# Kernel optimization log

Measured on AMD Instinct MI355X. Metric: run time of the kernel, lower is better.

The kernel has to match this reference:

```python
import jax, jax.numpy as jnp
import numpy as np

C = 32  # channel dim ('size' in the torch module)


def setup_inputs() -> dict:
    key = jax.random.key(0)
    ks = jax.random.split(key, 9)
    B, H, W = 8, 64, 512
    shape = (B, C, H, W)
    q = jax.random.normal(ks[0], shape, dtype=jnp.float32)
    k = jax.random.normal(ks[1], shape, dtype=jnp.float32)
    v = jax.random.normal(ks[2], shape, dtype=jnp.float32)
    s = 1.0 / np.sqrt(C)  # kaiming-uniform-ish scale for 1x1 conv
    wq = jax.random.uniform(ks[3], (C, C), jnp.float32, -s, s)
    bq = jax.random.uniform(ks[4], (C,), jnp.float32, -s, s)
    wk = jax.random.uniform(ks[5], (C, C), jnp.float32, -s, s)
    bk = jax.random.uniform(ks[6], (C,), jnp.float32, -s, s)
    wv = jax.random.uniform(ks[7], (C, C), jnp.float32, -s, s)
    bv = jax.random.uniform(ks[8], (C,), jnp.float32, -s, s)
    return {"q": q, "k": k, "v": v, "wq": wq, "bq": bq,
            "wk": wk, "bk": bk, "wv": wv, "bv": bv}


def _proj(x, w, b):
    # 1x1 conv on NCHW == per-pixel linear over channels; emit NHWC directly
    return jnp.einsum('oc,bchw->bhwo', w, x) + b


def reference(q, k, v, wq, bq, wk, bk, wv, bv):
    residual = q  # [B,C,H,W]
    qp = _proj(q, wq, bq)  # [B,H,W,C]
    kp = _proj(k, wk, bk)
    vp = _proj(v, wv, bv)
    # unnormalized attention over the W axis, batched over (B,H)
    attn = jnp.einsum('bhwc,bhxc->bhwx', qp, kp)        # [B,H,W,W]
    att = jnp.einsum('bhwx,bhxc->bhwc', attn, vp)       # [B,H,W,C]
    out = jnp.transpose(att, (0, 3, 1, 2)) + residual   # back to NCHW
    return out
```

## Files before the change

kernel.cpp:

```cpp
#include <hip/hip_runtime.h>
#include <hip/hip_bf16.h>

#define CH   32
#define WD   512
#define NH   64
#define CHST (NH * WD)
#define BST  (CH * CHST)
#define NST  36

typedef short bf16x8 __attribute__((ext_vector_type(8)));
typedef float f32x16 __attribute__((ext_vector_type(16)));
typedef float f32x8  __attribute__((ext_vector_type(8)));

__device__ __forceinline__ unsigned short f2bf(float f) {
  union { __hip_bfloat16 h; unsigned short u; } cv;
  cv.h = __float2bfloat16(f);
  return cv.u;
}
__device__ __forceinline__ float bf2f(unsigned short u) {
  return __uint_as_float(((unsigned int)u) << 16);
}
__device__ __forceinline__ unsigned int pk2(float lo_, float hi_) {
  return ((unsigned int)f2bf(hi_) << 16) | (unsigned int)f2bf(lo_);
}
__device__ __forceinline__ void swap32(unsigned int& a, unsigned int& b) {
  asm volatile("v_permlane32_swap_b32 %0, %1" : "+v"(a), "+v"(b));
}
union W4 { unsigned int u[4]; bf16x8 v; };

__device__ __forceinline__ void d2frag(const f32x16& d, W4& f0, W4& f1) {
  f0.u[0] = pk2(d[0], d[1]);   f0.u[1] = pk2(d[2],  d[3]);
  f0.u[2] = pk2(d[4], d[5]);   f0.u[3] = pk2(d[6],  d[7]);
  swap32(f0.u[0], f0.u[2]);    swap32(f0.u[1], f0.u[3]);
  f1.u[0] = pk2(d[8], d[9]);   f1.u[1] = pk2(d[10], d[11]);
  f1.u[2] = pk2(d[12], d[13]); f1.u[3] = pk2(d[14], d[15]);
  swap32(f1.u[0], f1.u[2]);    swap32(f1.u[1], f1.u[3]);
}
__device__ __forceinline__ float halfsum(float v) {
  return v + __shfl_xor(v, 32, 64);
}

__global__ __launch_bounds__(512, 4)
void fused_mha(const float* __restrict__ qg, const float* __restrict__ kg,
               const float* __restrict__ vg,
               const float* __restrict__ wqg, const float* __restrict__ bqg,
               const float* __restrict__ wkg, const float* __restrict__ bkg,
               const float* __restrict__ wvg, const float* __restrict__ bvg,
               float* __restrict__ outg)
{
  __shared__ float np[8][CH][NST];
  __shared__ float sp[8][2][CH];

  const int t = threadIdx.x, lane = t & 63, wid = t >> 6;
  const int lo = lane & 31, hi = lane >> 5;
  const int bh = blockIdx.x;
  const size_t base = (size_t)(bh >> 6) * BST + (size_t)(bh & 63) * WD;

  int rowr[16];
  #pragma unroll
  for (int r = 0; r < 16; ++r) rowr[r] = (r & 3) + 8 * (r >> 2) + 4 * hi;

  const float* krow = kg + base + (size_t)lo * CHST + 64 * wid + 8 * hi;
  const float* vrow = vg + base + (size_t)lo * CHST + 64 * wid + 8 * hi;
  f32x8 kf[4], vf[4];
  #pragma unroll
  for (int kk = 0; kk < 4; ++kk) {
    kf[kk] = *(const f32x8*)(krow + 16 * kk);
    vf[kk] = *(const f32x8*)(vrow + 16 * kk);
  }
  float qpf[32];
  #pragma unroll
  for (int it = 0; it < 2; ++it)
    #pragma unroll
    for (int s = 0; s < 2; ++s)
      #pragma unroll
      for (int j = 0; j < 8; ++j)
        qpf[16 * it + 8 * s + j] =
            qg[base + (size_t)(16 * s + 8 * hi + j) * CHST + 64 * wid + 32 * it + lo];

  bf16x8 wkA[2], wvA[2];
  {
    const float* wk_r = wkg + lo * CH + 8 * hi;
    const float* wv_r = wvg + lo * CH + 8 * hi;
    #pragma unroll
    for (int s = 0; s < 2; ++s)
      #pragma unroll
      for (int j = 0; j < 8; ++j) {
        wkA[s][j] = (short)f2bf(wk_r[16 * s + j]);
        wvA[s][j] = (short)f2bf(wv_r[16 * s + j]);
      }
  }

  f32x16 nacc;
  #pragma unroll
  for (int r = 0; r < 16; ++r) nacc[r] = 0.f;
  float psK = 0.f, psV = 0.f;
  #pragma unroll
  for (int kk = 0; kk < 4; ++kk) {
    W4 kb, vb;
    #pragma unroll
    for (int i = 0; i < 4; ++i) {
      kb.u[i] = pk2(kf[kk][2 * i], kf[kk][2 * i + 1]);
      vb.u[i] = pk2(vf[kk][2 * i], vf[kk][2 * i + 1]);
    }
    nacc = __builtin_amdgcn_mfma_f32_32x32x16_bf16(kb.v, vb.v, nacc, 0, 0, 0);
    #pragma unroll
    for (int j = 0; j < 8; ++j) { psK += kf[kk][j]; psV += vf[kk][j]; }
  }
  #pragma unroll
  for (int r = 0; r < 16; ++r) np[wid][rowr[r]][lo] = nacc[r];
  {
    const float sk = halfsum(psK), sv = halfsum(psV);
    if (hi == 0) { sp[wid][0][lo] = sk; sp[wid][1][lo] = sv; }
  }

  __syncthreads();

  {
    #pragma unroll
    for (int p = 0; p < 2; ++p) {
      const int e = t + 512 * p, o = e >> 5, c = e & 31;
      float s = 0.f;
      #pragma unroll
      for (int w = 0; w < 8; ++w) s += np[w][o][c];
      np[0][o][c] = s;
    }
    if (t < 64) {
      const int j = t >> 5, oo = t & 31;
      float s2 = 0.f;
      #pragma unroll
      for (int w = 0; w < 8; ++w) s2 += sp[w][j][oo];
      sp[0][j][oo] = s2;
    }
  }
  __syncthreads();

  bf16x8 wqA[2];
  {
    #pragma unroll
    for (int s = 0; s < 2; ++s)
      #pragma unroll
      for (int j = 0; j < 8; ++j)
        wqA[s][j] = (short)f2bf(wqg[(16 * s + 8 * hi + j) * CH + lo]);
  }
  float bkr[16], bqr[16];
  #pragma unroll
  for (int r = 0; r < 16; ++r) { bkr[r] = bkg[rowr[r]]; bqr[r] = bqg[rowr[r]]; }
  const float bvlo = bvg[lo];

  W4 NAh[2], NAl[2];
  #pragma unroll
  for (int s = 0; s < 2; ++s) {
    f32x8 nf = *(const f32x8*)&np[0][lo][16 * s + 8 * hi];
    #pragma unroll
    for (int i = 0; i < 4; ++i) {
      const float x = nf[2 * i], y = nf[2 * i + 1];
      const unsigned short hx = f2bf(x), hy = f2bf(y);
      NAh[s].u[i] = ((unsigned int)hy << 16) | hx;
      NAl[s].u[i] = pk2(x - bf2f(hx), y - bf2f(hy));
    }
  }
  f32x16 pacc;
  #pragma unroll
  for (int r = 0; r < 16; ++r) pacc[r] = 0.f;
  pacc = __builtin_amdgcn_mfma_f32_32x32x16_bf16(NAh[0].v, wvA[0], pacc, 0, 0, 0);
  pacc = __builtin_amdgcn_mfma_f32_32x32x16_bf16(NAh[1].v, wvA[1], pacc, 0, 0, 0);
  pacc = __builtin_amdgcn_mfma_f32_32x32x16_bf16(NAl[0].v, wvA[0], pacc, 0, 0, 0);
  pacc = __builtin_amdgcn_mfma_f32_32x32x16_bf16(NAl[1].v, wvA[1], pacc, 0, 0, 0);
  f32x16 pp;
  #pragma unroll
  for (int r = 0; r < 16; ++r) pp[r] = pacc[r] + sp[0][0][rowr[r]] * bvlo;
  float uprt = 0.f;
  #pragma unroll
  for (int s = 0; s < 2; ++s)
    #pragma unroll
    for (int j = 0; j < 8; ++j)
      uprt += bf2f((unsigned short)wvA[s][j]) * sp[0][1][16 * s + 8 * hi + j];
  const float uful = halfsum(uprt) + 512.f * bvlo;
  f32x16 pres;
  #pragma unroll
  for (int r = 0; r < 16; ++r) pres[r] = pp[r] - bf2f(f2bf(pp[r]));
  W4 pb0h, pb1h, pb0l, pb1l;
  d2frag(pp, pb0h, pb1h);
  d2frag(pres, pb0l, pb1l);
  f32x16 mac;
  #pragma unroll
  for (int r = 0; r < 16; ++r) mac[r] = bkr[r] * uful;
  mac = __builtin_amdgcn_mfma_f32_32x32x16_bf16(wkA[0], pb0h.v, mac, 0, 0, 0);
  mac = __builtin_amdgcn_mfma_f32_32x32x16_bf16(wkA[1], pb1h.v, mac, 0, 0, 0);
  mac = __builtin_amdgcn_mfma_f32_32x32x16_bf16(wkA[0], pb0l.v, mac, 0, 0, 0);
  mac = __builtin_amdgcn_mfma_f32_32x32x16_bf16(wkA[1], pb1l.v, mac, 0, 0, 0);
  W4 mb0, mb1;
  d2frag(mac, mb0, mb1);
  f32x16 gacc;
  #pragma unroll
  for (int r = 0; r < 16; ++r) gacc[r] = 0.f;
  gacc = __builtin_amdgcn_mfma_f32_32x32x16_bf16(wqA[0], mb0.v, gacc, 0, 0, 0);
  gacc = __builtin_amdgcn_mfma_f32_32x32x16_bf16(wqA[1], mb1.v, gacc, 0, 0, 0);
  #pragma unroll
  for (int r = 0; r < 16; ++r)
    if (rowr[r] == lo) gacc[r] += 1.f;
  float part = 0.f;
  #pragma unroll
  for (int r = 0; r < 16; ++r) part = fmaf(bqr[r], mac[r], part);
  const float gv = halfsum(part);
  W4 ga0, ga1;
  d2frag(gacc, ga0, ga1);
  float gsh[16];
  #pragma unroll
  for (int r = 0; r < 16; ++r) gsh[r] = __shfl(gv, rowr[r], 64);

  #pragma unroll
  for (int it = 0; it < 2; ++it) {
    const int x0 = 64 * wid + 32 * it;
    bf16x8 qb[2];
    #pragma unroll
    for (int s = 0; s < 2; ++s)
      #pragma unroll
      for (int j = 0; j < 8; ++j)
        qb[s][j] = (short)f2bf(qpf[16 * it + 8 * s + j]);
    f32x16 acc;
    #pragma unroll
    for (int r = 0; r < 16; ++r) acc[r] = gsh[r];
    acc = __builtin_amdgcn_mfma_f32_32x32x16_bf16(ga0.v, qb[0], acc, 0, 0, 0);
    acc = __builtin_amdgcn_mfma_f32_32x32x16_bf16(ga1.v, qb[1], acc, 0, 0, 0);
    #pragma unroll
    for (int r = 0; r < 16; ++r)
      outg[base + (size_t)rowr[r] * CHST + x0 + lo] = acc[r];
  }
}

extern "C" void kernel_launch(void* const* d_in, const int* in_sizes, int n_in,
                              void* d_out, int out_size, void* d_ws, size_t ws_size,
                              hipStream_t stream) {
  const float* q  = (const float*)d_in[0];
  const float* k  = (const float*)d_in[1];
  const float* v  = (const float*)d_in[2];
  const float* wq = (const float*)d_in[3];
  const float* bq = (const float*)d_in[4];
  const float* wk = (const float*)d_in[5];
  const float* bk = (const float*)d_in[6];
  const float* wv = (const float*)d_in[7];
  const float* bv = (const float*)d_in[8];
  float* out = (float*)d_out;

  (void)in_sizes; (void)n_in; (void)out_size; (void)d_ws; (void)ws_size;

  fused_mha<<<dim3(8 * 64), dim3(512), 0, stream>>>(q, k, v, wq, bq, wk, bk, wv, bv, out);
}
```

Before: 28.93 us.

## Process two (b,h) rows per block and prefetch second row's K/V during first

Result: slower. 36.01 us (+24.5%).

```diff
diff --git a/kernel.cpp b/kernel.cpp
--- a/kernel.cpp
+++ b/kernel.cpp
@@ -40,57 +40,11 @@
   return v + __shfl_xor(v, 32, 64);
 }
 
-__global__ __launch_bounds__(512, 4)
-void fused_mha(const float* __restrict__ qg, const float* __restrict__ kg,
-               const float* __restrict__ vg,
-               const float* __restrict__ wqg, const float* __restrict__ bqg,
-               const float* __restrict__ wkg, const float* __restrict__ bkg,
-               const float* __restrict__ wvg, const float* __restrict__ bvg,
-               float* __restrict__ outg)
+__device__ __forceinline__ void head_phase1(
+    const f32x8 kf[4], const f32x8 vf[4],
+    float (*nph)[CH][NST], float (*sph)[2][CH],
+    const int rowr[16], int lo, int hi, int wid)
 {
-  __shared__ float np[8][CH][NST];
-  __shared__ float sp[8][2][CH];
-
-  const int t = threadIdx.x, lane = t & 63, wid = t >> 6;
-  const int lo = lane & 31, hi = lane >> 5;
-  const int bh = blockIdx.x;
-  const size_t base = (size_t)(bh >> 6) * BST + (size_t)(bh & 63) * WD;
-
-  int rowr[16];
-  #pragma unroll
-  for (int r = 0; r < 16; ++r) rowr[r] = (r & 3) + 8 * (r >> 2) + 4 * hi;
-
-  const float* krow = kg + base + (size_t)lo * CHST + 64 * wid + 8 * hi;
-  const float* vrow = vg + base + (size_t)lo * CHST + 64 * wid + 8 * hi;
-  f32x8 kf[4], vf[4];
-  #pragma unroll
-  for (int kk = 0; kk < 4; ++kk) {
-    kf[kk] = *(const f32x8*)(krow + 16 * kk);
-    vf[kk] = *(const f32x8*)(vrow + 16 * kk);
-  }
-  float qpf[32];
-  #pragma unroll
-  for (int it = 0; it < 2; ++it)
-    #pragma unroll
-    for (int s = 0; s < 2; ++s)
-      #pragma unroll
-      for (int j = 0; j < 8; ++j)
-        qpf[16 * it + 8 * s + j] =
-            qg[base + (size_t)(16 * s + 8 * hi + j) * CHST + 64 * wid + 32 * it + lo];
-
-  bf16x8 wkA[2], wvA[2];
-  {
-    const float* wk_r = wkg + lo * CH + 8 * hi;
-    const float* wv_r = wvg + lo * CH + 8 * hi;
-    #pragma unroll
-    for (int s = 0; s < 2; ++s)
-      #pragma unroll
-      for (int j = 0; j < 8; ++j) {
-        wkA[s][j] = (short)f2bf(wk_r[16 * s + j]);
-        wvA[s][j] = (short)f2bf(wv_r[16 * s + j]);
-      }
-  }
-
   f32x16 nacc;
   #pragma unroll
   for (int r = 0; r < 16; ++r) nacc[r] = 0.f;
@@ -108,50 +62,40 @@
     for (int j = 0; j < 8; ++j) { psK += kf[kk][j]; psV += vf[kk][j]; }
   }
   #pragma unroll
-  for (int r = 0; r < 16; ++r) np[wid][rowr[r]][lo] = nacc[r];
-  {
-    const float sk = halfsum(psK), sv = halfsum(psV);
-    if (hi == 0) { sp[wid][0][lo] = sk; sp[wid][1][lo] = sv; }
-  }
-
+  for (int r = 0; r < 16; ++r) nph[wid][rowr[r]][lo] = nacc[r];
+  const float sk = halfsum(psK), sv = halfsum(psV);
+  if (hi == 0) { sph[wid][0][lo] = sk; sph[wid][1][lo] = sv; }
+}
+
+__device__ __forceinline__ void head_finish(
+    float (*nph)[CH][NST], float (*sph)[2][CH],
+    const bf16x8 wkA[2], const bf16x8 wvA[2], const bf16x8 wqA[2],
+    const float bkr[16], const float bqr[16], float bvlo,
+    const int rowr[16], int lo, int hi, int wid, int t,
+    const float qpf[32], float* __restrict__ outg, size_t base)
+{
   __syncthreads();
-
-  {
-    #pragma unroll
-    for (int p = 0; p < 2; ++p) {
-      const int e = t + 512 * p, o = e >> 5, c = e & 31;
-      float s = 0.f;
-      #pragma unroll
-      for (int w = 0; w < 8; ++w) s += np[w][o][c];
-      np[0][o][c] = s;
-    }
-    if (t < 64) {
-      const int j = t >> 5, oo = t & 31;
-      float s2 = 0.f;
-      #pragma unroll
-      for (int w = 0; w < 8; ++w) s2 += sp[w][j][oo];
-      sp[0][j][oo] = s2;
-    }
+  #pragma unroll
+  for (int p = 0; p < 2; ++p) {
+    const int e = t + 512 * p, o = e >> 5, c = e & 31;
+    float s = 0.f;
+    #pragma unroll
+    for (int w = 0; w < 8; ++w) s += nph[w][o][c];
+    nph[0][o][c] = s;
+  }
+  if (t < 64) {
+    const int j = t >> 5, oo = t & 31;
+    float s2 = 0.f;
+    #pragma unroll
+    for (int w = 0; w < 8; ++w) s2 += sph[w][j][oo];
+    sph[0][j][oo] = s2;
   }
   __syncthreads();
 
-  bf16x8 wqA[2];
-  {
-    #pragma unroll
-    for (int s = 0; s < 2; ++s)
-      #pragma unroll
-      for (int j = 0; j < 8; ++j)
-        wqA[s][j] = (short)f2bf(wqg[(16 * s + 8 * hi + j) * CH + lo]);
-  }
-  float bkr[16], bqr[16];
-  #pragma unroll
-  for (int r = 0; r < 16; ++r) { bkr[r] = bkg[rowr[r]]; bqr[r] = bqg[rowr[r]]; }
-  const float bvlo = bvg[lo];
-
   W4 NAh[2], NAl[2];
   #pragma unroll
   for (int s = 0; s < 2; ++s) {
-    f32x8 nf = *(const f32x8*)&np[0][lo][16 * s + 8 * hi];
+    f32x8 nf = *(const f32x8*)&nph[0][lo][16 * s + 8 * hi];
     #pragma unroll
     for (int i = 0; i < 4; ++i) {
       const float x = nf[2 * i], y = nf[2 * i + 1];
@@ -169,13 +113,13 @@
   pacc = __builtin_amdgcn_mfma_f32_32x32x16_bf16(NAl[1].v, wvA[1], pacc, 0, 0, 0);
   f32x16 pp;
   #pragma unroll
-  for (int r = 0; r < 16; ++r) pp[r] = pacc[r] + sp[0][0][rowr[r]] * bvlo;
+  for (int r = 0; r < 16; ++r) pp[r] = pacc[r] + sph[0][0][rowr[r]] * bvlo;
   float uprt = 0.f;
   #pragma unroll
   for (int s = 0; s < 2; ++s)
     #pragma unroll
     for (int j = 0; j < 8; ++j)
-      uprt += bf2f((unsigned short)wvA[s][j]) * sp[0][1][16 * s + 8 * hi + j];
+      uprt += bf2f((unsigned short)wvA[s][j]) * sph[0][1][16 * s + 8 * hi + j];
   const float uful = halfsum(uprt) + 512.f * bvlo;
   f32x16 pres;
   #pragma unroll
@@ -228,6 +172,94 @@
     for (int r = 0; r < 16; ++r)
       outg[base + (size_t)rowr[r] * CHST + x0 + lo] = acc[r];
   }
+}
+
+__global__ __launch_bounds__(512, 2)
+void fused_mha(const float* __restrict__ qg, const float* __restrict__ kg,
+               const float* __restrict__ vg,
+               const float* __restrict__ wqg, const float* __restrict__ bqg,
+               const float* __restrict__ wkg, const float* __restrict__ bkg,
+               const float* __restrict__ wvg, const float* __restrict__ bvg,
+               float* __restrict__ outg)
+{
+  __shared__ float np[2][8][CH][NST];
+  __shared__ float sp[2][8][2][CH];
+
+  const int t = threadIdx.x, lane = t & 63, wid = t >> 6;
+  const int lo = lane & 31, hi = lane >> 5;
+  const int bid = blockIdx.x;
+  const int bhA = 2 * bid, bhB = 2 * bid + 1;
+  const size_t baseA = (size_t)(bhA >> 6) * BST + (size_t)(bhA & 63) * WD;
+  const size_t baseB = (size_t)(bhB >> 6) * BST + (size_t)(bhB & 63) * WD;
+
+  int rowr[16];
+  #pragma unroll
+  for (int r = 0; r < 16; ++r) rowr[r] = (r & 3) + 8 * (r >> 2) + 4 * hi;
+
+  const float* krowA = kg + baseA + (size_t)lo * CHST + 64 * wid + 8 * hi;
+  const float* vrowA = vg + baseA + (size_t)lo * CHST + 64 * wid + 8 * hi;
+  f32x8 kfA[4], vfA[4];
+  #pragma unroll
+  for (int kk = 0; kk < 4; ++kk) {
+    kfA[kk] = *(const f32x8*)(krowA + 16 * kk);
+    vfA[kk] = *(const f32x8*)(vrowA + 16 * kk);
+  }
+  float qpfA[32];
+  #pragma unroll
+  for (int it = 0; it < 2; ++it)
+    #pragma unroll
+    for (int s = 0; s < 2; ++s)
+      #pragma unroll
+      for (int j = 0; j < 8; ++j)
+        qpfA[16 * it + 8 * s + j] =
+            qg[baseA + (size_t)(16 * s + 8 * hi + j) * CHST + 64 * wid + 32 * it + lo];
+
+  bf16x8 wkA[2], wvA[2], wqA[2];
+  {
+    const float* wk_r = wkg + lo * CH + 8 * hi;
+    const float* wv_r = wvg + lo * CH + 8 * hi;
+    #pragma unroll
+    for (int s = 0; s < 2; ++s)
+      #pragma unroll
+      for (int j = 0; j < 8; ++j) {
+        wkA[s][j] = (short)f2bf(wk_r[16 * s + j]);
+        wvA[s][j] = (short)f2bf(wv_r[16 * s + j]);
+        wqA[s][j] = (short)f2bf(wqg[(16 * s + 8 * hi + j) * CH + lo]);
+      }
+  }
+  float bkr[16], bqr[16];
+  #pragma unroll
+  for (int r = 0; r < 16; ++r) { bkr[r] = bkg[rowr[r]]; bqr[r] = bqg[rowr[r]]; }
+  const float bvlo = bvg[lo];
+
+  head_phase1(kfA, vfA, np[0], sp[0], rowr, lo, hi, wid);
+
+  const float* krowB = kg + baseB + (size_t)lo * CHST + 64 * wid + 8 * hi;
+  const float* vrowB = vg + baseB + (size_t)lo * CHST + 64 * wid + 8 * hi;
+  f32x8 kfB[4], vfB[4];
+  #pragma unroll
+  for (int kk = 0; kk < 4; ++kk) {
+    kfB[kk] = *(const f32x8*)(krowB + 16 * kk);
+    vfB[kk] = *(const f32x8*)(vrowB + 16 * kk);
+  }
+
+  head_finish(np[0], sp[0], wkA, wvA, wqA, bkr, bqr, bvlo,
+              rowr, lo, hi, wid, t, qpfA, outg, baseA);
+
+  float qpfB[32];
+  #pragma unroll
+  for (int it = 0; it < 2; ++it)
+    #pragma unroll
+    for (int s = 0; s < 2; ++s)
+      #pragma unroll
+      for (int j = 0; j < 8; ++j)
+        qpfB[16 * it + 8 * s + j] =
+            qg[baseB + (size_t)(16 * s + 8 * hi + j) * CHST + 64 * wid + 32 * it + lo];
+
+  head_phase1(kfB, vfB, np[1], sp[1], rowr, lo, hi, wid);
+
+  head_finish(np[1], sp[1], wkA, wvA, wqA, bkr, bqr, bvlo,
+              rowr, lo, hi, wid, t, qpfB, outg, baseB);
 }
 
 extern "C" void kernel_launch(void* const* d_in, const int* in_sizes, int n_in,
@@ -246,5 +278,5 @@
 
   (void)in_sizes; (void)n_in; (void)out_size; (void)d_ws; (void)ws_size;
 
-  fused_mha<<<dim3(8 * 64), dim3(512), 0, stream>>>(q, k, v, wq, bq, wk, bk, wv, bv, out);
-}
+  fused_mha<<<dim3(256), dim3(512), 0, stream>>>(q, k, v, wq, bq, wk, bk, wv, bv, out);
+}
```

## Split each (b,h) row across two blocks with global atomic reduction and flag sync

Applied to the files above, without the earlier changes.

Result: slower. 112.8 us (+289.9%).

```diff
diff --git a/kernel.cpp b/kernel.cpp
--- a/kernel.cpp
+++ b/kernel.cpp
@@ -40,28 +40,32 @@
   return v + __shfl_xor(v, 32, 64);
 }
 
-__global__ __launch_bounds__(512, 4)
+__global__ __launch_bounds__(256, 4)
 void fused_mha(const float* __restrict__ qg, const float* __restrict__ kg,
                const float* __restrict__ vg,
                const float* __restrict__ wqg, const float* __restrict__ bqg,
                const float* __restrict__ wkg, const float* __restrict__ bkg,
                const float* __restrict__ wvg, const float* __restrict__ bvg,
-               float* __restrict__ outg)
+               float* __restrict__ outg,
+               float* __restrict__ Nws, float* __restrict__ Sws,
+               unsigned int* __restrict__ flagws)
 {
-  __shared__ float np[8][CH][NST];
-  __shared__ float sp[8][2][CH];
+  __shared__ float np[4][CH][NST];
+  __shared__ float sp[4][2][CH];
 
   const int t = threadIdx.x, lane = t & 63, wid = t >> 6;
   const int lo = lane & 31, hi = lane >> 5;
-  const int bh = blockIdx.x;
+  const int bid = blockIdx.x;
+  const int bh = bid >> 1, half = bid & 1;
   const size_t base = (size_t)(bh >> 6) * BST + (size_t)(bh & 63) * WD;
+  const int xw = 256 * half + 64 * wid;
 
   int rowr[16];
   #pragma unroll
   for (int r = 0; r < 16; ++r) rowr[r] = (r & 3) + 8 * (r >> 2) + 4 * hi;
 
-  const float* krow = kg + base + (size_t)lo * CHST + 64 * wid + 8 * hi;
-  const float* vrow = vg + base + (size_t)lo * CHST + 64 * wid + 8 * hi;
+  const float* krow = kg + base + (size_t)lo * CHST + xw + 8 * hi;
+  const float* vrow = vg + base + (size_t)lo * CHST + xw + 8 * hi;
   f32x8 kf[4], vf[4];
   #pragma unroll
   for (int kk = 0; kk < 4; ++kk) {
@@ -76,9 +80,9 @@
       #pragma unroll
       for (int j = 0; j < 8; ++j)
         qpf[16 * it + 8 * s + j] =
-            qg[base + (size_t)(16 * s + 8 * hi + j) * CHST + 64 * wid + 32 * it + lo];
-
-  bf16x8 wkA[2], wvA[2];
+            qg[base + (size_t)(16 * s + 8 * hi + j) * CHST + xw + 32 * it + lo];
+
+  bf16x8 wkA[2], wvA[2], wqA[2];
   {
     const float* wk_r = wkg + lo * CH + 8 * hi;
     const float* wv_r = wvg + lo * CH + 8 * hi;
@@ -88,65 +92,71 @@
       for (int j = 0; j < 8; ++j) {
         wkA[s][j] = (short)f2bf(wk_r[16 * s + j]);
         wvA[s][j] = (short)f2bf(wv_r[16 * s + j]);
+        wqA[s][j] = (short)f2bf(wqg[(16 * s + 8 * hi + j) * CH + lo]);
       }
   }
-
-  f32x16 nacc;
-  #pragma unroll
-  for (int r = 0; r < 16; ++r) nacc[r] = 0.f;
-  float psK = 0.f, psV = 0.f;
-  #pragma unroll
-  for (int kk = 0; kk < 4; ++kk) {
-    W4 kb, vb;
-    #pragma unroll
-    for (int i = 0; i < 4; ++i) {
-      kb.u[i] = pk2(kf[kk][2 * i], kf[kk][2 * i + 1]);
-      vb.u[i] = pk2(vf[kk][2 * i], vf[kk][2 * i + 1]);
+  float bkr[16], bqr[16];
+  #pragma unroll
+  for (int r = 0; r < 16; ++r) { bkr[r] = bkg[rowr[r]]; bqr[r] = bqg[rowr[r]]; }
+  const float bvlo = bvg[lo];
+
+  {
+    f32x16 nacc;
+    #pragma unroll
+    for (int r = 0; r < 16; ++r) nacc[r] = 0.f;
+    float psK = 0.f, psV = 0.f;
+    #pragma unroll
+    for (int kk = 0; kk < 4; ++kk) {
+      W4 kb, vb;
+      #pragma unroll
+      for (int i = 0; i < 4; ++i) {
+        kb.u[i] = pk2(kf[kk][2 * i], kf[kk][2 * i + 1]);
+        vb.u[i] = pk2(vf[kk][2 * i], vf[kk][2 * i + 1]);
+      }
+      nacc = __builtin_amdgcn_mfma_f32_32x32x16_bf16(kb.v, vb.v, nacc, 0, 0, 0);
+      #pragma unroll
+      for (int j = 0; j < 8; ++j) { psK += kf[kk][j]; psV += vf[kk][j]; }
     }
-    nacc = __builtin_amdgcn_mfma_f32_32x32x16_bf16(kb.v, vb.v, nacc, 0, 0, 0);
-    #pragma unroll
-    for (int j = 0; j < 8; ++j) { psK += kf[kk][j]; psV += vf[kk][j]; }
-  }
-  #pragma unroll
-  for (int r = 0; r < 16; ++r) np[wid][rowr[r]][lo] = nacc[r];
-  {
+    #pragma unroll
+    for (int r = 0; r < 16; ++r) np[wid][rowr[r]][lo] = nacc[r];
     const float sk = halfsum(psK), sv = halfsum(psV);
     if (hi == 0) { sp[wid][0][lo] = sk; sp[wid][1][lo] = sv; }
   }
-
-  __syncthreads();
-
-  {
-    #pragma unroll
-    for (int p = 0; p < 2; ++p) {
-      const int e = t + 512 * p, o = e >> 5, c = e & 31;
-      float s = 0.f;
-      #pragma unroll
-      for (int w = 0; w < 8; ++w) s += np[w][o][c];
-      np[0][o][c] = s;
-    }
-    if (t < 64) {
-      const int j = t >> 5, oo = t & 31;
-      float s2 = 0.f;
-      #pragma unroll
-      for (int w = 0; w < 8; ++w) s2 += sp[w][j][oo];
-      sp[0][j][oo] = s2;
-    }
-  }
-  __syncthreads();
-
-  bf16x8 wqA[2];
-  {
-    #pragma unroll
-    for (int s = 0; s < 2; ++s)
-      #pragma unroll
-      for (int j = 0; j < 8; ++j)
-        wqA[s][j] = (short)f2bf(wqg[(16 * s + 8 * hi + j) * CH + lo]);
-  }
-  float bkr[16], bqr[16];
-  #pragma unroll
-  for (int r = 0; r < 16; ++r) { bkr[r] = bkg[rowr[r]]; bqr[r] = bqg[rowr[r]]; }
-  const float bvlo = bvg[lo];
+  __syncthreads();
+
+  #pragma unroll
+  for (int p = 0; p < 4; ++p) {
+    const int e = t + 256 * p, o = e >> 5, c = e & 31;
+    const float s = np[0][o][c] + np[1][o][c] + np[2][o][c] + np[3][o][c];
+    atomicAdd(&Nws[(size_t)bh * 1024 + e], s);
+  }
+  if (t < 64) {
+    const int j = t >> 5, oo = t & 31;
+    const float s2 = sp[0][j][oo] + sp[1][j][oo] + sp[2][j][oo] + sp[3][j][oo];
+    atomicAdd(&Sws[(size_t)bh * 64 + t], s2);
+  }
+  __syncthreads();
+
+  if (t == 0) {
+    __threadfence();
+    __hip_atomic_fetch_add(&flagws[bh], 1u, __ATOMIC_RELEASE, __HIP_MEMORY_SCOPE_AGENT);
+    while (__hip_atomic_load(&flagws[bh], __ATOMIC_ACQUIRE, __HIP_MEMORY_SCOPE_AGENT) < 2u)
+      __builtin_amdgcn_s_sleep(2);
+  }
+  __syncthreads();
+
+  #pragma unroll
+  for (int p = 0; p < 4; ++p) {
+    const int e = t + 256 * p;
+    np[0][e >> 5][e & 31] =
+        __hip_atomic_load(&Nws[(size_t)bh * 1024 + e], __ATOMIC_RELAXED,
+                          __HIP_MEMORY_SCOPE_AGENT);
+  }
+  if (t < 64)
+    sp[0][t >> 5][t & 31] =
+        __hip_atomic_load(&Sws[(size_t)bh * 64 + t], __ATOMIC_RELAXED,
+                          __HIP_MEMORY_SCOPE_AGENT);
+  __syncthreads();
 
   W4 NAh[2], NAl[2];
   #pragma unroll
@@ -212,7 +222,7 @@
 
   #pragma unroll
   for (int it = 0; it < 2; ++it) {
-    const int x0 = 64 * wid + 32 * it;
+    const int x0 = xw + 32 * it;
     bf16x8 qb[2];
     #pragma unroll
     for (int s = 0; s < 2; ++s)
@@ -244,7 +254,14 @@
   const float* bv = (const float*)d_in[8];
   float* out = (float*)d_out;
 
-  (void)in_sizes; (void)n_in; (void)out_size; (void)d_ws; (void)ws_size;
-
-  fused_mha<<<dim3(8 * 64), dim3(512), 0, stream>>>(q, k, v, wq, bq, wk, bk, wv, bv, out);
-}
+  float* Nws = (float*)d_ws;
+  float* Sws = Nws + 512 * 1024;
+  unsigned int* flagws = (unsigned int*)(Sws + 512 * 64);
+  const size_t ws_needed = (size_t)(512 * 1024 + 512 * 64 + 512) * 4;
+
+  (void)in_sizes; (void)n_in; (void)out_size; (void)ws_size;
+
+  hipMemsetAsync(d_ws, 0, ws_needed, stream);
+  fused_mha<<<dim3(1024), dim3(256), 0, stream>>>(q, k, v, wq, bq, wk, bk, wv, bv,
+                                                  out, Nws, Sws, flagws);
+}
```

## Split fused attention into producer and consumer blocks linked by global flags

Applied to the files above, without the earlier changes.

Result: slower. 57.47 us (+98.6%).

```diff
diff --git a/kernel.cpp b/kernel.cpp
--- a/kernel.cpp
+++ b/kernel.cpp
@@ -41,192 +41,228 @@
 }
 
 __global__ __launch_bounds__(512, 4)
-void fused_mha(const float* __restrict__ qg, const float* __restrict__ kg,
-               const float* __restrict__ vg,
-               const float* __restrict__ wqg, const float* __restrict__ bqg,
-               const float* __restrict__ wkg, const float* __restrict__ bkg,
-               const float* __restrict__ wvg, const float* __restrict__ bvg,
-               float* __restrict__ outg)
+void fused_mha_pc(const float* __restrict__ qg, const float* __restrict__ kg,
+                  const float* __restrict__ vg,
+                  const float* __restrict__ wqg, const float* __restrict__ bqg,
+                  const float* __restrict__ wkg, const float* __restrict__ bkg,
+                  const float* __restrict__ wvg, const float* __restrict__ bvg,
+                  float* __restrict__ outg,
+                  unsigned int* __restrict__ GWu, float* __restrict__ gwf,
+                  unsigned int* __restrict__ flagws)
 {
   __shared__ float np[8][CH][NST];
   __shared__ float sp[8][2][CH];
 
   const int t = threadIdx.x, lane = t & 63, wid = t >> 6;
   const int lo = lane & 31, hi = lane >> 5;
-  const int bh = blockIdx.x;
+  const int bid = blockIdx.x;
+  const bool producer = bid < 512;
+  const int bh = producer ? bid : bid - 512;
   const size_t base = (size_t)(bh >> 6) * BST + (size_t)(bh & 63) * WD;
 
   int rowr[16];
   #pragma unroll
   for (int r = 0; r < 16; ++r) rowr[r] = (r & 3) + 8 * (r >> 2) + 4 * hi;
 
-  const float* krow = kg + base + (size_t)lo * CHST + 64 * wid + 8 * hi;
-  const float* vrow = vg + base + (size_t)lo * CHST + 64 * wid + 8 * hi;
-  f32x8 kf[4], vf[4];
-  #pragma unroll
-  for (int kk = 0; kk < 4; ++kk) {
-    kf[kk] = *(const f32x8*)(krow + 16 * kk);
-    vf[kk] = *(const f32x8*)(vrow + 16 * kk);
-  }
-  float qpf[32];
-  #pragma unroll
-  for (int it = 0; it < 2; ++it)
+  if (producer) {
+    const float* krow = kg + base + (size_t)lo * CHST + 64 * wid + 8 * hi;
+    const float* vrow = vg + base + (size_t)lo * CHST + 64 * wid + 8 * hi;
+    f32x8 kf[4], vf[4];
+    #pragma unroll
+    for (int kk = 0; kk < 4; ++kk) {
+      kf[kk] = *(const f32x8*)(krow + 16 * kk);
+      vf[kk] = *(const f32x8*)(vrow + 16 * kk);
+    }
+    bf16x8 wkA[2], wvA[2], wqA[2];
+    {
+      const float* wk_r = wkg + lo * CH + 8 * hi;
+      const float* wv_r = wvg + lo * CH + 8 * hi;
+      #pragma unroll
+      for (int s = 0; s < 2; ++s)
+        #pragma unroll
+        for (int j = 0; j < 8; ++j) {
+          wkA[s][j] = (short)f2bf(wk_r[16 * s + j]);
+          wvA[s][j] = (short)f2bf(wv_r[16 * s + j]);
+          wqA[s][j] = (short)f2bf(wqg[(16 * s + 8 * hi + j) * CH + lo]);
+        }
+    }
+    float bkr[16], bqr[16];
+    #pragma unroll
+    for (int r = 0; r < 16; ++r) { bkr[r] = bkg[rowr[r]]; bqr[r] = bqg[rowr[r]]; }
+    const float bvlo = bvg[lo];
+
+    f32x16 nacc;
+    #pragma unroll
+    for (int r = 0; r < 16; ++r) nacc[r] = 0.f;
+    float psK = 0.f, psV = 0.f;
+    #pragma unroll
+    for (int kk = 0; kk < 4; ++kk) {
+      W4 kb, vb;
+      #pragma unroll
+      for (int i = 0; i < 4; ++i) {
+        kb.u[i] = pk2(kf[kk][2 * i], kf[kk][2 * i + 1]);
+        vb.u[i] = pk2(vf[kk][2 * i], vf[kk][2 * i + 1]);
+      }
+      nacc = __builtin_amdgcn_mfma_f32_32x32x16_bf16(kb.v, vb.v, nacc, 0, 0, 0);
+      #pragma unroll
+      for (int j = 0; j < 8; ++j) { psK += kf[kk][j]; psV += vf[kk][j]; }
+    }
+    #pragma unroll
+    for (int r = 0; r < 16; ++r) np[wid][rowr[r]][lo] = nacc[r];
+    {
+      const float sk = halfsum(psK), sv = halfsum(psV);
+      if (hi == 0) { sp[wid][0][lo] = sk; sp[wid][1][lo] = sv; }
+    }
+    __syncthreads();
+
+    {
+      #pragma unroll
+      for (int p = 0; p < 2; ++p) {
+        const int e = t + 512 * p, o = e >> 5, c = e & 31;
+        float s = 0.f;
+        #pragma unroll
+        for (int w = 0; w < 8; ++w) s += np[w][o][c];
+        np[0][o][c] = s;
+      }
+      if (t < 64) {
+        const int j = t >> 5, oo = t & 31;
+        float s2 = 0.f;
+        #pragma unroll
+        for (int w = 0; w < 8; ++w) s2 += sp[w][j][oo];
+        sp[0][j][oo] = s2;
+      }
+    }
+    __syncthreads();
+
+    W4 NAh[2], NAl[2];
+    #pragma unroll
+    for (int s = 0; s < 2; ++s) {
+      f32x8 nf = *(const f32x8*)&np[0][lo][16 * s + 8 * hi];
+      #pragma unroll
+      for (int i = 0; i < 4; ++i) {
+        const float x = nf[2 * i], y = nf[2 * i + 1];
+        const unsigned short hx = f2bf(x), hy = f2bf(y);
+        NAh[s].u[i] = ((unsigned int)hy << 16) | hx;
+        NAl[s].u[i] = pk2(x - bf2f(hx), y - bf2f(hy));
+      }
+    }
+    f32x16 pacc;
+    #pragma unroll
+    for (int r = 0; r < 16; ++r) pacc[r] = 0.f;
+    pacc = __builtin_amdgcn_mfma_f32_32x32x16_bf16(NAh[0].v, wvA[0], pacc, 0, 0, 0);
+    pacc = __builtin_amdgcn_mfma_f32_32x32x16_bf16(NAh[1].v, wvA[1], pacc, 0, 0, 0);
+    pacc = __builtin_amdgcn_mfma_f32_32x32x16_bf16(NAl[0].v, wvA[0], pacc, 0, 0, 0);
+    pacc = __builtin_amdgcn_mfma_f32_32x32x16_bf16(NAl[1].v, wvA[1], pacc, 0, 0, 0);
+    f32x16 pp;
+    #pragma unroll
+    for (int r = 0; r < 16; ++r) pp[r] = pacc[r] + sp[0][0][rowr[r]] * bvlo;
+    float uprt = 0.f;
     #pragma unroll
     for (int s = 0; s < 2; ++s)
       #pragma unroll
       for (int j = 0; j < 8; ++j)
-        qpf[16 * it + 8 * s + j] =
-            qg[base + (size_t)(16 * s + 8 * hi + j) * CHST + 64 * wid + 32 * it + lo];
-
-  bf16x8 wkA[2], wvA[2];
-  {
-    const float* wk_r = wkg + lo * CH + 8 * hi;
-    const float* wv_r = wvg + lo * CH + 8 * hi;
-    #pragma unroll
-    for (int s = 0; s < 2; ++s)
-      #pragma unroll
-      for (int j = 0; j < 8; ++j) {
-        wkA[s][j] = (short)f2bf(wk_r[16 * s + j]);
-        wvA[s][j] = (short)f2bf(wv_r[16 * s + j]);
-      }
-  }
-
-  f32x16 nacc;
-  #pragma unroll
-  for (int r = 0; r < 16; ++r) nacc[r] = 0.f;
-  float psK = 0.f, psV = 0.f;
-  #pragma unroll
-  for (int kk = 0; kk < 4; ++kk) {
-    W4 kb, vb;
+        uprt += bf2f((unsigned short)wvA[s][j]) * sp[0][1][16 * s + 8 * hi + j];
+    const float uful = halfsum(uprt) + 512.f * bvlo;
+    f32x16 pres;
+    #pragma unroll
+    for (int r = 0; r < 16; ++r) pres[r] = pp[r] - bf2f(f2bf(pp[r]));
+    W4 pb0h, pb1h, pb0l, pb1l;
+    d2frag(pp, pb0h, pb1h);
+    d2frag(pres, pb0l, pb1l);
+    f32x16 mac;
+    #pragma unroll
+    for (int r = 0; r < 16; ++r) mac[r] = bkr[r] * uful;
+    mac = __builtin_amdgcn_mfma_f32_32x32x16_bf16(wkA[0], pb0h.v, mac, 0, 0, 0);
+    mac = __builtin_amdgcn_mfma_f32_32x32x16_bf16(wkA[1], pb1h.v, mac, 0, 0, 0);
+    mac = __builtin_amdgcn_mfma_f32_32x32x16_bf16(wkA[0], pb0l.v, mac, 0, 0, 0);
+    mac = __builtin_amdgcn_mfma_f32_32x32x16_bf16(wkA[1], pb1l.v, mac, 0, 0, 0);
+    W4 mb0, mb1;
+    d2frag(mac, mb0, mb1);
+    f32x16 gacc;
+    #pragma unroll
+    for (int r = 0; r < 16; ++r) gacc[r] = 0.f;
+    gacc = __builtin_amdgcn_mfma_f32_32x32x16_bf16(wqA[0], mb0.v, gacc, 0, 0, 0);
+    gacc = __builtin_amdgcn_mfma_f32_32x32x16_bf16(wqA[1], mb1.v, gacc, 0, 0, 0);
+    #pragma unroll
+    for (int r = 0; r < 16; ++r)
+      if (rowr[r] == lo) gacc[r] += 1.f;
+    float part = 0.f;
+    #pragma unroll
+    for (int r = 0; r < 16; ++r) part = fmaf(bqr[r], mac[r], part);
+    const float gv = halfsum(part);
+    W4 ga0, ga1;
+    d2frag(gacc, ga0, ga1);
+
+    if (wid == 0) {
+      const int li = hi * 32 + lo;
+      unsigned int* gp = GWu + (size_t)bh * 512 + li * 4;
+      #pragma unroll
+      for (int i = 0; i < 4; ++i) {
+        __hip_atomic_store(gp + i, ga0.u[i], __ATOMIC_RELAXED,
+                           __HIP_MEMORY_SCOPE_AGENT);
+        __hip_atomic_store(gp + 256 + i, ga1.u[i], __ATOMIC_RELAXED,
+                           __HIP_MEMORY_SCOPE_AGENT);
+      }
+      if (hi == 0)
+        __hip_atomic_store((unsigned int*)&gwf[bh * 32 + lo], __float_as_uint(gv),
+                           __ATOMIC_RELAXED, __HIP_MEMORY_SCOPE_AGENT);
+      if (t == 0)
+        __hip_atomic_store(&flagws[bh], 1u, __ATOMIC_RELEASE,
+                           __HIP_MEMORY_SCOPE_AGENT);
+    }
+  } else {
+    float qpf[32];
+    #pragma unroll
+    for (int it = 0; it < 2; ++it)
+      #pragma unroll
+      for (int s = 0; s < 2; ++s)
+        #pragma unroll
+        for (int j = 0; j < 8; ++j)
+          qpf[16 * it + 8 * s + j] =
+              qg[base + (size_t)(16 * s + 8 * hi + j) * CHST + 64 * wid + 32 * it + lo];
+
+    if (t == 0) {
+      while (__hip_atomic_load(&flagws[bh], __ATOMIC_ACQUIRE,
+                               __HIP_MEMORY_SCOPE_AGENT) == 0u)
+        __builtin_amdgcn_s_sleep(8);
+    }
+    __syncthreads();
+
+    const int li = hi * 32 + lo;
+    W4 ga0, ga1;
+    const unsigned int* gp = GWu + (size_t)bh * 512 + li * 4;
     #pragma unroll
     for (int i = 0; i < 4; ++i) {
-      kb.u[i] = pk2(kf[kk][2 * i], kf[kk][2 * i + 1]);
-      vb.u[i] = pk2(vf[kk][2 * i], vf[kk][2 * i + 1]);
-    }
-    nacc = __builtin_amdgcn_mfma_f32_32x32x16_bf16(kb.v, vb.v, nacc, 0, 0, 0);
-    #pragma unroll
-    for (int j = 0; j < 8; ++j) { psK += kf[kk][j]; psV += vf[kk][j]; }
-  }
-  #pragma unroll
-  for (int r = 0; r < 16; ++r) np[wid][rowr[r]][lo] = nacc[r];
-  {
-    const float sk = halfsum(psK), sv = halfsum(psV);
-    if (hi == 0) { sp[wid][0][lo] = sk; sp[wid][1][lo] = sv; }
-  }
-
-  __syncthreads();
-
-  {
-    #pragma unroll
-    for (int p = 0; p < 2; ++p) {
-      const int e = t + 512 * p, o = e >> 5, c = e & 31;
-      float s = 0.f;
-      #pragma unroll
-      for (int w = 0; w < 8; ++w) s += np[w][o][c];
-      np[0][o][c] = s;
-    }
-    if (t < 64) {
-      const int j = t >> 5, oo = t & 31;
-      float s2 = 0.f;
-      #pragma unroll
-      for (int w = 0; w < 8; ++w) s2 += sp[w][j][oo];
-      sp[0][j][oo] = s2;
-    }
-  }
-  __syncthreads();
-
-  bf16x8 wqA[2];
-  {
-    #pragma unroll
-    for (int s = 0; s < 2; ++s)
-      #pragma unroll
-      for (int j = 0; j < 8; ++j)
-        wqA[s][j] = (short)f2bf(wqg[(16 * s + 8 * hi + j) * CH + lo]);
-  }
-  float bkr[16], bqr[16];
-  #pragma unroll
-  for (int r = 0; r < 16; ++r) { bkr[r] = bkg[rowr[r]]; bqr[r] = bqg[rowr[r]]; }
-  const float bvlo = bvg[lo];
-
-  W4 NAh[2], NAl[2];
-  #pragma unroll
-  for (int s = 0; s < 2; ++s) {
-    f32x8 nf = *(const f32x8*)&np[0][lo][16 * s + 8 * hi];
-    #pragma unroll
-    for (int i = 0; i < 4; ++i) {
-      const float x = nf[2 * i], y = nf[2 * i + 1];
-      const unsigned short hx = f2bf(x), hy = f2bf(y);
-      NAh[s].u[i] = ((unsigned int)hy << 16) | hx;
-      NAl[s].u[i] = pk2(x - bf2f(hx), y - bf2f(hy));
-    }
-  }
-  f32x16 pacc;
-  #pragma unroll
-  for (int r = 0; r < 16; ++r) pacc[r] = 0.f;
-  pacc = __builtin_amdgcn_mfma_f32_32x32x16_bf16(NAh[0].v, wvA[0], pacc, 0, 0, 0);
-  pacc = __builtin_amdgcn_mfma_f32_32x32x16_bf16(NAh[1].v, wvA[1], pacc, 0, 0, 0);
-  pacc = __builtin_amdgcn_mfma_f32_32x32x16_bf16(NAl[0].v, wvA[0], pacc, 0, 0, 0);
-  pacc = __builtin_amdgcn_mfma_f32_32x32x16_bf16(NAl[1].v, wvA[1], pacc, 0, 0, 0);
-  f32x16 pp;
-  #pragma unroll
-  for (int r = 0; r < 16; ++r) pp[r] = pacc[r] + sp[0][0][rowr[r]] * bvlo;
-  float uprt = 0.f;
-  #pragma unroll
-  for (int s = 0; s < 2; ++s)
-    #pragma unroll
-    for (int j = 0; j < 8; ++j)
-      uprt += bf2f((unsigned short)wvA[s][j]) * sp[0][1][16 * s + 8 * hi + j];
-  const float uful = halfsum(uprt) + 512.f * bvlo;
-  f32x16 pres;
-  #pragma unroll
-  for (int r = 0; r < 16; ++r) pres[r] = pp[r] - bf2f(f2bf(pp[r]));
-  W4 pb0h, pb1h, pb0l, pb1l;
-  d2frag(pp, pb0h, pb1h);
-  d2frag(pres, pb0l, pb1l);
-  f32x16 mac;
-  #pragma unroll
-  for (int r = 0; r < 16; ++r) mac[r] = bkr[r] * uful;
-  mac = __builtin_amdgcn_mfma_f32_32x32x16_bf16(wkA[0], pb0h.v, mac, 0, 0, 0);
-  mac = __builtin_amdgcn_mfma_f32_32x32x16_bf16(wkA[1], pb1h.v, mac, 0, 0, 0);
-  mac = __builtin_amdgcn_mfma_f32_32x32x16_bf16(wkA[0], pb0l.v, mac, 0, 0, 0);
-  mac = __builtin_amdgcn_mfma_f32_32x32x16_bf16(wkA[1], pb1l.v, mac, 0, 0, 0);
-  W4 mb0, mb1;
-  d2frag(mac, mb0, mb1);
-  f32x16 gacc;
-  #pragma unroll
-  for (int r = 0; r < 16; ++r) gacc[r] = 0.f;
-  gacc = __builtin_amdgcn_mfma_f32_32x32x16_bf16(wqA[0], mb0.v, gacc, 0, 0, 0);
-  gacc = __builtin_amdgcn_mfma_f32_32x32x16_bf16(wqA[1], mb1.v, gacc, 0, 0, 0);
-  #pragma unroll
-  for (int r = 0; r < 16; ++r)
-    if (rowr[r] == lo) gacc[r] += 1.f;
-  float part = 0.f;
-  #pragma unroll
-  for (int r = 0; r < 16; ++r) part = fmaf(bqr[r], mac[r], part);
-  const float gv = halfsum(part);
-  W4 ga0, ga1;
-  d2frag(gacc, ga0, ga1);
-  float gsh[16];
-  #pragma unroll
-  for (int r = 0; r < 16; ++r) gsh[r] = __shfl(gv, rowr[r], 64);
-
-  #pragma unroll
-  for (int it = 0; it < 2; ++it) {
-    const int x0 = 64 * wid + 32 * it;
-    bf16x8 qb[2];
-    #pragma unroll
-    for (int s = 0; s < 2; ++s)
-      #pragma unroll
-      for (int j = 0; j < 8; ++j)
-        qb[s][j] = (short)f2bf(qpf[16 * it + 8 * s + j]);
-    f32x16 acc;
-    #pragma unroll
-    for (int r = 0; r < 16; ++r) acc[r] = gsh[r];
-    acc = __builtin_amdgcn_mfma_f32_32x32x16_bf16(ga0.v, qb[0], acc, 0, 0, 0);
-    acc = __builtin_amdgcn_mfma_f32_32x32x16_bf16(ga1.v, qb[1], acc, 0, 0, 0);
+      ga0.u[i] = __hip_atomic_load(gp + i, __ATOMIC_RELAXED,
+                                   __HIP_MEMORY_SCOPE_AGENT);
+      ga1.u[i] = __hip_atomic_load(gp + 256 + i, __ATOMIC_RELAXED,
+                                   __HIP_MEMORY_SCOPE_AGENT);
+    }
+    float gsh[16];
     #pragma unroll
     for (int r = 0; r < 16; ++r)
-      outg[base + (size_t)rowr[r] * CHST + x0 + lo] = acc[r];
+      gsh[r] = __uint_as_float(
+          __hip_atomic_load((const unsigned int*)&gwf[bh * 32 + rowr[r]],
+                            __ATOMIC_RELAXED, __HIP_MEMORY_SCOPE_AGENT));
+
+    #pragma unroll
+    for (int it = 0; it < 2; ++it) {
+      const int x0 = 64 * wid + 32 * it;
+      bf16x8 qb[2];
+      #pragma unroll
+      for (int s = 0; s < 2; ++s)
+        #pragma unroll
+        for (int j = 0; j < 8; ++j)
+          qb[s][j] = (short)f2bf(qpf[16 * it + 8 * s + j]);
+      f32x16 acc;
+      #pragma unroll
+      for (int r = 0; r < 16; ++r) acc[r] = gsh[r];
+      acc = __builtin_amdgcn_mfma_f32_32x32x16_bf16(ga0.v, qb[0], acc, 0, 0, 0);
+      acc = __builtin_amdgcn_mfma_f32_32x32x16_bf16(ga1.v, qb[1], acc, 0, 0, 0);
+      #pragma unroll
+      for (int r = 0; r < 16; ++r)
+        outg[base + (size_t)rowr[r] * CHST + x0 + lo] = acc[r];
+    }
   }
 }
 
@@ -244,7 +280,13 @@
   const float* bv = (const float*)d_in[8];
   float* out = (float*)d_out;
 
-  (void)in_sizes; (void)n_in; (void)out_size; (void)d_ws; (void)ws_size;
-
-  fused_mha<<<dim3(8 * 64), dim3(512), 0, stream>>>(q, k, v, wq, bq, wk, bk, wv, bv, out);
-}
+  unsigned int* GWu = (unsigned int*)d_ws;
+  float* gwf = (float*)(GWu + 512 * 512);
+  unsigned int* flagws = (unsigned int*)(gwf + 512 * 32);
+
+  (void)in_sizes; (void)n_in; (void)out_size; (void)ws_size;
+
+  hipMemsetAsync(flagws, 0, 512 * sizeof(unsigned int), stream);
+  fused_mha_pc<<<dim3(1024), dim3(512), 0, stream>>>(q, k, v, wq, bq, wk, bk, wv, bv,
+                                                     out, GWu, gwf, flagws);
+}
```
